# Kernel tuning notes

Hardware: AMD Instinct MI355X
Metric: run time of the kernel (lower is better)

Reference implementation:

```python
import jax, jax.numpy as jnp
import numpy as np

NUM_HEAVY = 1024
N_ITERS = 50
FETCH_K_RATIO = 9.0 / 8.0
EPS = 1.0


def rmsnorm(x, gamma):
    scale = gamma.shape[0] ** 0.5
    normed = x / jnp.maximum(jnp.linalg.norm(x, axis=-1, keepdims=True), 1e-12)
    return normed * scale * gamma


def feedforward(x, gamma, w1, b1, w2, b2):
    h = rmsnorm(x, gamma)
    h = jax.nn.gelu(h @ w1.T + b1, approximate=False)
    return h @ w2.T + b2


def coor_descent(s, n_iters, k, eps):
    # s: [b, n] router logits; faithful to lucidrains coor_descent (no mask, const eps)
    logk = jnp.log(jnp.asarray(k, s.dtype))
    a0 = jnp.zeros_like(s[..., :1])
    b0 = -s

    def body(carry, _):
        a, b = carry
        a = eps * (logk - jax.nn.logsumexp((s + b) / eps, axis=-1, keepdims=True))
        b = -jax.nn.relu(s + a)
        return (a, b), None

    (a, b), _ = jax.lax.scan(body, (a0, b0), None, length=n_iters)
    return jnp.exp((s + a + b) / eps)


def setup_inputs() -> dict:
    key = jax.random.key(0)
    ks = jax.random.split(key, 12)
    b, n, dim = 8, 8192, 1024
    d_light, d_heavy = int(dim * 0.5), dim * 4

    def lin(k, dout, din):
        bound = 1.0 / np.sqrt(din)
        k1, k2 = jax.random.split(k)
        w = jax.random.uniform(k1, (dout, din), jnp.float32, -bound, bound)
        bb = jax.random.uniform(k2, (dout,), jnp.float32, -bound, bound)
        return w, bb

    x = jax.random.normal(ks[0], (b, n, dim), jnp.float32)
    routing_token = jax.random.normal(ks[1], (dim,), jnp.float32)
    w1_l, b1_l = lin(ks[2], d_light, dim)
    w2_l, b2_l = lin(ks[3], dim, d_light)
    w1_h, b1_h = lin(ks[4], d_heavy, dim)
    w2_h, b2_h = lin(ks[5], dim, d_heavy)
    return dict(
        x=x, routing_token=routing_token,
        gamma_l=jnp.ones((dim,), jnp.float32), w1_l=w1_l, b1_l=b1_l, w2_l=w2_l, b2_l=b2_l,
        gamma_h=jnp.ones((dim,), jnp.float32), w1_h=w1_h, b1_h=b1_h, w2_h=w2_h, b2_h=b2_h,
    )


def reference(x, routing_token, gamma_l, w1_l, b1_l, w2_l, b2_l,
              gamma_h, w1_h, b1_h, w2_h, b2_h):
    b, n, dim = x.shape
    # light branch on all tokens
    light_out = feedforward(x, gamma_l, w1_l, b1_l, w2_l, b2_l)

    # router (coor_descent, num_routing_tokens=1, no mask)
    s = jnp.einsum('bnd,d->bn', x, routing_token)
    effective_k = min(NUM_HEAVY * FETCH_K_RATIO, n)
    scores = coor_descent(s, N_ITERS, effective_k, EPS)
    selected_scores, selected_indices = jax.lax.top_k(scores, NUM_HEAVY)
    # straight-through: value -> 1, grad flows through selected_scores
    selected_scores = selected_scores + jax.lax.stop_gradient(1.0 - selected_scores)

    # gather -> heavy FFN -> scale -> scatter back
    routed = jnp.take_along_axis(x, selected_indices[..., None], axis=1)  # [b, k, d]
    routed_out = feedforward(routed, gamma_h, w1_h, b1_h, w2_h, b2_h)
    routed_out = routed_out * selected_scores[..., None]

    batch_range = jnp.arange(b)[:, None]
    heavy_out = jnp.zeros_like(x).at[batch_range, selected_indices].set(routed_out)
    return light_out + heavy_out
```

## Files before the change

kernel.cpp:

```cpp
#include <hip/hip_runtime.h>
#include <cstdint>
#include <cstddef>


#define DEV __device__ __forceinline__

typedef __bf16 bf16x8 __attribute__((ext_vector_type(8)));
typedef float floatx4 __attribute__((ext_vector_type(4)));

DEV unsigned short f2bf(float f) {
  unsigned int u = __float_as_uint(f);
  u += 0x7FFFu + ((u >> 16) & 1u);
  return (unsigned short)(u >> 16);
}

__global__ __launch_bounds__(256) void convw_gamma_kernel(
    const float* __restrict__ w, const float* __restrict__ gamma,
    unsigned short* __restrict__ wb, int n) {
  int i = blockIdx.x * 256 + threadIdx.x;
  if (i < n) wb[i] = f2bf(w[i] * gamma[i & 1023]);
}
__global__ __launch_bounds__(256) void convw_kernel(
    const float* __restrict__ w, unsigned short* __restrict__ wb, int n) {
  int i = blockIdx.x * 256 + threadIdx.x;
  if (i < n) wb[i] = f2bf(w[i]);
}

__global__ __launch_bounds__(256) void prep_kernel(
    const float* __restrict__ x, const float* __restrict__ rt,
    unsigned short* __restrict__ xn, double* __restrict__ s) {
  const int token = blockIdx.x;
  const int tid = threadIdx.x;
  const float4 v = ((const float4*)(x + (size_t)token * 1024))[tid];
  const float4 r = ((const float4*)rt)[tid];
  float ss = v.x * v.x + v.y * v.y + v.z * v.z + v.w * v.w;
  double dot = (double)v.x * r.x + (double)v.y * r.y + (double)v.z * r.z + (double)v.w * r.w;
  const int wave = tid >> 6, lane = tid & 63;
#pragma unroll
  for (int off = 32; off; off >>= 1) {
    ss += __shfl_down(ss, off);
    dot += __shfl_down(dot, off);
  }
  __shared__ float ssr[4];
  __shared__ double dr[4];
  __shared__ float scale_sh;
  if (lane == 0) { ssr[wave] = ss; dr[wave] = dot; }
  __syncthreads();
  if (tid == 0) {
    float tot = ssr[0] + ssr[1] + ssr[2] + ssr[3];
    scale_sh = 32.0f / fmaxf(sqrtf(tot), 1e-12f);
    s[token] = dr[0] + dr[1] + dr[2] + dr[3];
  }
  __syncthreads();
  const float sc = scale_sh;
  ushort4 o;
  o.x = f2bf(v.x * sc); o.y = f2bf(v.y * sc);
  o.z = f2bf(v.z * sc); o.w = f2bf(v.w * sc);
  ((ushort4*)(xn + (size_t)token * 1024))[tid] = o;
}

__global__ __launch_bounds__(1024) void coor_kernel(
    const double* __restrict__ s, double* __restrict__ a_out) {
  const int b = blockIdx.x, tid = threadIdx.x;
  const int wave = tid >> 6, lane = tid & 63;
  __shared__ double red[16];
  __shared__ double bcast;
  const double* sb = s + (size_t)b * 8192;
  double sv[8], es[8];
#pragma unroll
  for (int i = 0; i < 8; ++i) {
    sv[i] = sb[tid * 8 + i];
    es[i] = exp(sv[i]);
  }
  const double logk = log(1152.0);
  double a = logk - log(8192.0);
  for (int it = 0; it < 49; ++it) {
    const double th = -a;
    const double eth = exp(th);
    double sum = 0.0;
#pragma unroll
    for (int i = 0; i < 8; ++i) sum += (sv[i] < th) ? es[i] : eth;
#pragma unroll
    for (int off = 32; off; off >>= 1) sum += __shfl_down(sum, off);
    if (lane == 0) red[wave] = sum;
    __syncthreads();
    if (tid == 0) {
      double t = 0.0;
      for (int i = 0; i < 16; ++i) t += red[i];
      bcast = logk - log(t);
    }
    __syncthreads();
    a = bcast;
  }
  if (tid == 0) a_out[b] = a;
}

__global__ __launch_bounds__(1024) void select_kernel(
    const double* __restrict__ s, const double* __restrict__ a_in,
    int* __restrict__ sel) {
  const int b = blockIdx.x, tid = threadIdx.x;
  const int wave = tid >> 6, lane = tid & 63;
  const double a = a_in[b];
  const double* sb = s + (size_t)b * 8192;
  const int base = tid * 8;
  double sv[8];
  bool ind[8];
  int cnt = 0;
#pragma unroll
  for (int i = 0; i < 8; ++i) {
    sv[i] = sb[base + i];
    ind[i] = (sv[i] + a >= 0.0);
    cnt += ind[i] ? 1 : 0;
  }
  __shared__ int sc[1024];
  sc[tid] = cnt;
  __syncthreads();
  for (int off = 1; off < 1024; off <<= 1) {
    int v = sc[tid];
    int add = (tid >= off) ? sc[tid - off] : 0;
    __syncthreads();
    sc[tid] = v + add;
    __syncthreads();
  }
  const int m = sc[1023];
  int p = sc[tid] - cnt;
#pragma unroll
  for (int i = 0; i < 8; ++i) {
    if (ind[i]) {
      if (p < 1024) sel[b * 1024 + p] = base + i;
      ++p;
    }
  }
  if (m >= 1024) return;

  __shared__ double rv[16];
  __shared__ int ri[16];
  __shared__ int gsel;
  bool taken[8] = {false, false, false, false, false, false, false, false};
  const int need = 1024 - m;
  for (int t = 0; t < need; ++t) {
    double bvv = -1.0e300;
    int bi = 0x7FFFFFFF;
#pragma unroll
    for (int i = 0; i < 8; ++i)
      if (!ind[i] && !taken[i] && sv[i] > bvv) { bvv = sv[i]; bi = base + i; }
#pragma unroll
    for (int off = 32; off; off >>= 1) {
      double ov = __shfl_down(bvv, off);
      int oi = __shfl_down(bi, off);
      if (ov > bvv || (ov == bvv && oi < bi)) { bvv = ov; bi = oi; }
    }
    if (lane == 0) { rv[wave] = bvv; ri[wave] = bi; }
    __syncthreads();
    if (tid == 0) {
      double mv = rv[0]; int mi = ri[0];
      for (int i = 1; i < 16; ++i)
        if (rv[i] > mv || (rv[i] == mv && ri[i] < mi)) { mv = rv[i]; mi = ri[i]; }
      gsel = mi;
      sel[b * 1024 + m + t] = mi;
    }
    __syncthreads();
    const int g = gsel;
    if (g >= base && g < base + 8) taken[g - base] = true;
    __syncthreads();
  }
}

__global__ __launch_bounds__(256) void gather_kernel(
    const unsigned short* __restrict__ xn, const int* __restrict__ sel,
    unsigned short* __restrict__ xg) {
  const int r = blockIdx.x;
  const int b = r >> 10;
  const int idx = sel[r];
  const uint2* src = (const uint2*)(xn + ((size_t)(b << 13) + idx) * 1024);
  uint2* dst = (uint2*)(xg + (size_t)r * 1024);
  dst[threadIdx.x] = src[threadIdx.x];
}


enum {
  RA00 = 0,      RA01 = 16384,  RA10 = 32768,  RA11 = 49152,
  RB00 = 65536,  RB01 = 81920,  RB10 = 98304,  RB11 = 114688
};

#define VMCNT(n) asm volatile("s_waitcnt vmcnt(" #n ")" ::: "memory")
#define BARR() __builtin_amdgcn_s_barrier()
#define SCHED0() __builtin_amdgcn_sched_barrier(0)

#define STG_A(DST, KOFF)                                                      \
  do {                                                                        \
    _Pragma("unroll") for (int r_ = 0; r_ < 2; ++r_)                          \
        __builtin_amdgcn_global_load_lds(                                     \
            (__attribute__((address_space(1))) void*)(Asrc[r_] + (KOFF)),     \
            (__attribute__((address_space(3))) void*)(sh + (DST) + r_ * 8192 +\
                                                     ldsW),                   \
            16, 0, 0);                                                        \
  } while (0)

#define STG_B(DST, KOFF)                                                      \
  do {                                                                        \
    _Pragma("unroll") for (int r_ = 0; r_ < 2; ++r_)                          \
        __builtin_amdgcn_global_load_lds(                                     \
            (__attribute__((address_space(1))) void*)(Bsrc[r_] + (KOFF)),     \
            (__attribute__((address_space(3))) void*)(sh + (DST) + r_ * 8192 +\
                                                     ldsW),                   \
            16, 0, 0);                                                        \
  } while (0)

#define PH(RAOFF, RBOFF, MH, LOADB, STG)                                      \
  do {                                                                        \
    bf16x8 a_[4];                                                             \
    _Pragma("unroll") for (int f_ = 0; f_ < 4; ++f_) a_[f_] =                 \
        *(const bf16x8*)(sh + (RAOFF) + f_ * 2048 + rbA);                     \
    if (LOADB) {                                                              \
      _Pragma("unroll") for (int n_ = 0; n_ < 4; ++n_) bq[n_] =               \
          *(const bf16x8*)(sh + (RBOFF) + n_ * 2048 + rbB);                   \
    }                                                                         \
    STG;                                                                      \
    __builtin_amdgcn_s_setprio(1);                                            \
    _Pragma("unroll") for (int f_ = 0; f_ < 4; ++f_)                          \
        _Pragma("unroll") for (int n_ = 0; n_ < 4; ++n_) acc[(MH) + f_][n_] = \
            __builtin_amdgcn_mfma_f32_16x16x32_bf16(a_[f_], bq[n_],           \
                                                    acc[(MH) + f_][n_], 0, 0, \
                                                    0);                       \
    __builtin_amdgcn_s_setprio(0);                                            \
  } while (0)

#define ITER_FULL(I)                                                          \
  do {                                                                        \
    const int ks4 = ((2 * (I) + 1) << 6) + 32;                                \
    const int ks1 = ((2 * (I) + 2) << 6);                                     \
    const int ks2 = ks1 + 32;                                                 \
    const int ks3 = ((2 * (I) + 3) << 6);                                     \
    PH(RA00, RB00, 0, 1, STG_A(RA11, ks4));                                   \
    PH(RA00 + 8192, RB00, 4, 0, STG_B(RB11, ks4));                            \
    VMCNT(8); BARR(); SCHED0();                                               \
    PH(RA01, RB01, 0, 1, STG_A(RA00, ks1));                                   \
    PH(RA01 + 8192, RB01, 4, 0, STG_B(RB00, ks1));                            \
    VMCNT(8); BARR(); SCHED0();                                               \
    PH(RA10, RB10, 0, 1, STG_A(RA01, ks2));                                   \
    PH(RA10 + 8192, RB10, 4, 0, STG_B(RB01, ks2));                            \
    VMCNT(8); BARR(); SCHED0();                                               \
    PH(RA11, RB11, 0, 1, STG_A(RA10, ks3));                                   \
    PH(RA11 + 8192, RB11, 4, 0, STG_B(RB10, ks3));                            \
    VMCNT(8); BARR(); SCHED0();                                               \
  } while (0)

#define ITER_LAST(I)                                                          \
  do {                                                                        \
    const int ks4 = ((2 * (I) + 1) << 6) + 32;                                \
    PH(RA00, RB00, 0, 1, STG_A(RA11, ks4));                                   \
    PH(RA00 + 8192, RB00, 4, 0, STG_B(RB11, ks4));                            \
    VMCNT(8); BARR(); SCHED0();                                               \
    PH(RA01, RB01, 0, 1, );                                                   \
    PH(RA01 + 8192, RB01, 4, 0, );                                            \
    VMCNT(4); BARR(); SCHED0();                                               \
    PH(RA10, RB10, 0, 1, );                                                   \
    PH(RA10 + 8192, RB10, 4, 0, );                                            \
    VMCNT(0); BARR(); SCHED0();                                               \
    PH(RA11, RB11, 0, 1, );                                                   \
    PH(RA11 + 8192, RB11, 4, 0, );                                            \
  } while (0)

template <int MODE>
__global__ __launch_bounds__(512, 2) void gemm8p_kernel(
    const unsigned short* __restrict__ A, const unsigned short* __restrict__ B,
    const float* __restrict__ bias, float* __restrict__ outF,
    unsigned short* __restrict__ outH, int M, int N, int K) {
  __shared__ alignas(16) char sh[131072];

  const int tiles_n = N >> 8;
  const int nwg = gridDim.x;
  const int bid = blockIdx.x;
  const int cpx = nwg >> 3;
  const int swz = (bid & 7) * cpx + (bid >> 3);
  const int bm = swz / tiles_n, bn = swz - bm * tiles_n;

  const int tid = threadIdx.x;
  const int wave = tid >> 6, lane = tid & 63;
  const int l16 = lane & 15, q = lane >> 4;
  const int wm = wave >> 2, wn = wave & 3;

  const int slA = (((wm * 4 + q) ^ (l16 & 7)) << 4);
  const int slB = ((((wn >> 1) * 4 + q) ^ (l16 & 7)) << 4);
  const int rbA = l16 * 128 + slA;
  const int rbB = (wn & 1) * 8192 + l16 * 128 + slB;

  const int ssrc = (tid & 7) ^ ((tid >> 3) & 7);
  const int hfold = ssrc >> 2, chunk = ssrc & 3;
  const unsigned short* Asrc[2];
  const unsigned short* Bsrc[2];
#pragma unroll
  for (int r = 0; r < 2; ++r) {
    const int grow = r * 64 + (tid >> 3) + hfold * 128;
    Asrc[r] = A + (size_t)(bm * 256 + grow) * K + chunk * 8;
    Bsrc[r] = B + (size_t)(bn * 256 + grow) * K + chunk * 8;
  }
  const int ldsW = wave * 1024;

  floatx4 acc[8][4];
#pragma unroll
  for (int i = 0; i < 8; ++i)
#pragma unroll
    for (int j = 0; j < 4; ++j) acc[i][j] = 0.0f;
  bf16x8 bq[4];

  STG_A(RA00, 0);  STG_B(RB00, 0);
  STG_A(RA01, 32); STG_B(RB01, 32);
  STG_A(RA10, 64); STG_B(RB10, 64);
  VMCNT(8); BARR(); SCHED0();

  const int NI = K >> 7;
#pragma unroll 1
  for (int i = 0; i < NI - 1; ++i) ITER_FULL(i);
  ITER_LAST(NI - 1);

  const int gm0 = bm * 256 + wm * 128 + q * 4;
  const int gn0 = bn * 256 + wn * 64 + l16;
#pragma unroll
  for (int m = 0; m < 8; ++m) {
#pragma unroll
    for (int n = 0; n < 4; ++n) {
      const int col = gn0 + n * 16;
      const float bv = bias[col];
#pragma unroll
      for (int r = 0; r < 4; ++r) {
        const int row = gm0 + m * 16 + r;
        float v = acc[m][n][r] + bv;
        if (MODE == 0) {
          float g = 0.5f * v * (1.0f + erff(v * 0.70710678118654752f));
          outH[(size_t)row * N + col] = f2bf(g);
        } else {
          outF[(size_t)row * N + col] = v;
        }
      }
    }
  }
}

template <int MODE>
__global__ __launch_bounds__(256, 3) void gemm_bt_kernel(
    const unsigned short* __restrict__ A, const unsigned short* __restrict__ B,
    const float* __restrict__ bias, float* __restrict__ outF,
    unsigned short* __restrict__ outH, const int* __restrict__ sel,
    int M, int N, int K) {
  constexpr int BK = 32;
  __shared__ alignas(16) unsigned short As[128 * BK];
  __shared__ alignas(16) unsigned short Bs[128 * BK];
  const int tiles_n = N >> 7;
  int bid = blockIdx.x;
  if ((gridDim.x & 7) == 0) {
    bid = (bid & 7) * (gridDim.x >> 3) + (bid >> 3);
  }
  const int bm = bid / tiles_n;
  const int bn = bid - bm * tiles_n;
  const int tid = threadIdx.x;
  const int wave = tid >> 6, lane = tid & 63;
  const int quad = lane >> 4, l16 = lane & 15;
  const int wm = (wave >> 1) << 6;
  const int wn = (wave & 1) << 6;

  floatx4 acc[4][4];
#pragma unroll
  for (int i = 0; i < 4; ++i)
#pragma unroll
    for (int j = 0; j < 4; ++j) acc[i][j] = 0.0f;

  const int sr = tid >> 2;
  const int scol = (tid & 3) << 3;
  const unsigned short* Ag = A + ((size_t)(bm * 128 + sr)) * K + scol;
  const unsigned short* Bg = B + ((size_t)(bn * 128 + sr)) * K + scol;
  const size_t rowstep = (size_t)64 * K;
  char* AsB = (char*)&As[0];
  char* BsB = (char*)&Bs[0];
  const int ldsbase = wave * 1024;

  for (int k0 = 0; k0 < K; k0 += BK) {
#pragma unroll
    for (int iss = 0; iss < 2; ++iss) {
      __builtin_amdgcn_global_load_lds(
          (__attribute__((address_space(1))) void*)(Ag + iss * rowstep + k0),
          (__attribute__((address_space(3))) void*)(AsB + ldsbase + iss * 4096), 16, 0, 0);
      __builtin_amdgcn_global_load_lds(
          (__attribute__((address_space(1))) void*)(Bg + iss * rowstep + k0),
          (__attribute__((address_space(3))) void*)(BsB + ldsbase + iss * 4096), 16, 0, 0);
    }
    __syncthreads();
    bf16x8 af[4], bfr[4];
#pragma unroll
    for (int mi = 0; mi < 4; ++mi)
      af[mi] = *(const bf16x8*)(As + (wm + mi * 16 + l16) * BK + quad * 8);
#pragma unroll
    for (int ni = 0; ni < 4; ++ni)
      bfr[ni] = *(const bf16x8*)(Bs + (wn + ni * 16 + l16) * BK + quad * 8);
#pragma unroll
    for (int mi = 0; mi < 4; ++mi)
#pragma unroll
      for (int ni = 0; ni < 4; ++ni)
        acc[mi][ni] = __builtin_amdgcn_mfma_f32_16x16x32_bf16(af[mi], bfr[ni], acc[mi][ni], 0, 0, 0);
    __syncthreads();
  }

  const int gm0 = bm * 128 + wm + quad * 4;
  const int gn0 = bn * 128 + wn + l16;
#pragma unroll
  for (int mi = 0; mi < 4; ++mi) {
#pragma unroll
    for (int ni = 0; ni < 4; ++ni) {
      const int col = gn0 + ni * 16;
      const float bv = bias[col];
#pragma unroll
      for (int r = 0; r < 4; ++r) {
        const int row = gm0 + mi * 16 + r;
        float v = acc[mi][ni][r] + bv;
        if (MODE == 0) {
          float g = 0.5f * v * (1.0f + erff(v * 0.70710678118654752f));
          outH[(size_t)row * N + col] = f2bf(g);
        } else if (MODE == 1) {
          outF[(size_t)row * N + col] = v;
        } else {
          const int idx = sel[row];
          const size_t op = (((size_t)((row >> 10) << 13) + idx) << 10) + col;
          outF[op] += v;
        }
      }
    }
  }
}

extern "C" void kernel_launch(void* const* d_in, const int* in_sizes, int n_in,
                              void* d_out, int out_size, void* d_ws, size_t ws_size,
                              hipStream_t stream) {
  const float* x    = (const float*)d_in[0];
  const float* rt   = (const float*)d_in[1];
  const float* g_l  = (const float*)d_in[2];
  const float* w1_l = (const float*)d_in[3];
  const float* b1_l = (const float*)d_in[4];
  const float* w2_l = (const float*)d_in[5];
  const float* b2_l = (const float*)d_in[6];
  const float* g_h  = (const float*)d_in[7];
  const float* w1_h = (const float*)d_in[8];
  const float* b1_h = (const float*)d_in[9];
  const float* w2_h = (const float*)d_in[10];
  const float* b2_h = (const float*)d_in[11];
  float* out = (float*)d_out;

  char* ws = (char*)d_ws;
  size_t off = 0;
  auto alloc = [&](size_t bytes) -> char* {
    char* p = ws + off;
    off += (bytes + 255) & ~(size_t)255;
    return p;
  };
  unsigned short* xn  = (unsigned short*)alloc((size_t)65536 * 1024 * 2);
  double* s           = (double*)alloc((size_t)65536 * 8);
  double* a_out       = (double*)alloc(256);
  int* sel            = (int*)alloc(8192 * 4);
  unsigned short* w1l = (unsigned short*)alloc((size_t)512 * 1024 * 2);
  unsigned short* w2l = (unsigned short*)alloc((size_t)1024 * 512 * 2);
  unsigned short* w1h = (unsigned short*)alloc((size_t)4096 * 1024 * 2);
  unsigned short* w2h = (unsigned short*)alloc((size_t)1024 * 4096 * 2);
  unsigned short* xg  = (unsigned short*)alloc((size_t)8192 * 1024 * 2);
  unsigned short* h1  = (unsigned short*)alloc((size_t)33554432 * 2);
  if (off > ws_size) return;

  convw_gamma_kernel<<<524288 / 256, 256, 0, stream>>>(w1_l, g_l, w1l, 524288);
  convw_kernel<<<524288 / 256, 256, 0, stream>>>(w2_l, w2l, 524288);
  convw_gamma_kernel<<<4194304 / 256, 256, 0, stream>>>(w1_h, g_h, w1h, 4194304);
  convw_kernel<<<4194304 / 256, 256, 0, stream>>>(w2_h, w2h, 4194304);

  prep_kernel<<<65536, 256, 0, stream>>>(x, rt, xn, s);
  coor_kernel<<<8, 1024, 0, stream>>>(s, a_out);
  select_kernel<<<8, 1024, 0, stream>>>(s, a_out, sel);
  gather_kernel<<<8192, 256, 0, stream>>>(xn, sel, xg);

  gemm8p_kernel<0><<<256 * 2, 512, 0, stream>>>(xn, w1l, b1_l, nullptr, h1, 65536, 512, 1024);
  gemm8p_kernel<1><<<256 * 4, 512, 0, stream>>>(h1, w2l, b2_l, out, nullptr, 65536, 1024, 512);
  gemm8p_kernel<0><<<32 * 16, 512, 0, stream>>>(xg, w1h, b1_h, nullptr, h1, 8192, 4096, 1024);
  gemm_bt_kernel<2><<<64 * 8, 256, 0, stream>>>(h1, w2h, b2_h, out, nullptr, sel, 8192, 1024, 4096);
}
```

Baseline: 951.6 us.

## Fuse gather into heavy GEMM, split-K heavy down-proj, merge heavy output into light epilogue

The heavy branch now loads its selected token rows straight from xn through per-row gathered A pointers, so the separate gather kernel goes away. The heavy down-projection moves from the slow 128-tile kernel to the pipelined 256-tile kernel with a 2-way split-K into two fp32 buffers. The light second GEMM's epilogue then adds those partials using an inverse selection map, replacing the read-modify-write scatter and reordering the branches. This costs extra global traffic for the fp32 partials and an invsel write per token.

```diff
diff --git a/kernel.cpp b/kernel.cpp
--- a/kernel.cpp
+++ b/kernel.cpp
@@ -97,7 +97,7 @@
 
 __global__ __launch_bounds__(1024) void select_kernel(
     const double* __restrict__ s, const double* __restrict__ a_in,
-    int* __restrict__ sel) {
+    int* __restrict__ sel, int* __restrict__ invsel) {
   const int b = blockIdx.x, tid = threadIdx.x;
   const int wave = tid >> 6, lane = tid & 63;
   const double a = a_in[b];
@@ -126,10 +126,12 @@
   int p = sc[tid] - cnt;
 #pragma unroll
   for (int i = 0; i < 8; ++i) {
+    int w = -1;
     if (ind[i]) {
-      if (p < 1024) sel[b * 1024 + p] = base + i;
+      if (p < 1024) { sel[b * 1024 + p] = base + i; w = p; }
       ++p;
     }
+    invsel[b * 8192 + base + i] = w;
   }
   if (m >= 1024) return;
 
@@ -158,23 +160,13 @@
         if (rv[i] > mv || (rv[i] == mv && ri[i] < mi)) { mv = rv[i]; mi = ri[i]; }
       gsel = mi;
       sel[b * 1024 + m + t] = mi;
+      invsel[b * 8192 + mi] = m + t;
     }
     __syncthreads();
     const int g = gsel;
     if (g >= base && g < base + 8) taken[g - base] = true;
     __syncthreads();
   }
-}
-
-__global__ __launch_bounds__(256) void gather_kernel(
-    const unsigned short* __restrict__ xn, const int* __restrict__ sel,
-    unsigned short* __restrict__ xg) {
-  const int r = blockIdx.x;
-  const int b = r >> 10;
-  const int idx = sel[r];
-  const uint2* src = (const uint2*)(xn + ((size_t)(b << 13) + idx) * 1024);
-  uint2* dst = (uint2*)(xg + (size_t)r * 1024);
-  dst[threadIdx.x] = src[threadIdx.x];
 }
 
 
@@ -262,11 +254,13 @@
     PH(RA11 + 8192, RB11, 4, 0, );                                            \
   } while (0)
 
-template <int MODE>
+template <int MODE, bool SELA>
 __global__ __launch_bounds__(512, 2) void gemm8p_kernel(
     const unsigned short* __restrict__ A, const unsigned short* __restrict__ B,
     const float* __restrict__ bias, float* __restrict__ outF,
-    unsigned short* __restrict__ outH, int M, int N, int K) {
+    unsigned short* __restrict__ outH, const int* __restrict__ sel,
+    const float* __restrict__ hA, const float* __restrict__ hB,
+    float* __restrict__ outF2, int M, int N, int K) {
   __shared__ alignas(16) char sh[131072];
 
   const int tiles_n = N >> 8;
@@ -274,7 +268,12 @@
   const int bid = blockIdx.x;
   const int cpx = nwg >> 3;
   const int swz = (bid & 7) * cpx + (bid >> 3);
-  const int bm = swz / tiles_n, bn = swz - bm * tiles_n;
+
+  int tile = swz, ksplit = 0;
+  if (MODE == 3) { ksplit = swz >= (nwg >> 1); tile = swz & ((nwg >> 1) - 1); }
+  const int Kloop = (MODE == 3) ? (K >> 1) : K;
+  const int kbase = (MODE == 3) ? ksplit * (K >> 1) : 0;
+  const int bm = tile / tiles_n, bn = tile - bm * tiles_n;
 
   const int tid = threadIdx.x;
   const int wave = tid >> 6, lane = tid & 63;
@@ -292,9 +291,15 @@
   const unsigned short* Bsrc[2];
 #pragma unroll
   for (int r = 0; r < 2; ++r) {
-    const int grow = r * 64 + (tid >> 3) + hfold * 128;
-    Asrc[r] = A + (size_t)(bm * 256 + grow) * K + chunk * 8;
-    Bsrc[r] = B + (size_t)(bn * 256 + grow) * K + chunk * 8;
+    const int growA = bm * 256 + r * 64 + (tid >> 3) + hfold * 128;
+    const int growB = bn * 256 + r * 64 + (tid >> 3) + hfold * 128;
+    if (SELA) {
+      const int bb = growA >> 10;
+      Asrc[r] = A + ((size_t)((bb << 13) + sel[growA])) * K + kbase + chunk * 8;
+    } else {
+      Asrc[r] = A + (size_t)growA * K + kbase + chunk * 8;
+    }
+    Bsrc[r] = B + (size_t)growB * K + kbase + chunk * 8;
   }
   const int ldsW = wave * 1024;
 
@@ -310,19 +315,20 @@
   STG_A(RA10, 64); STG_B(RB10, 64);
   VMCNT(8); BARR(); SCHED0();
 
-  const int NI = K >> 7;
+  const int NI = Kloop >> 7;
 #pragma unroll 1
   for (int i = 0; i < NI - 1; ++i) ITER_FULL(i);
   ITER_LAST(NI - 1);
 
   const int gm0 = bm * 256 + wm * 128 + q * 4;
   const int gn0 = bn * 256 + wn * 64 + l16;
+  float* const oF = (MODE == 3 && ksplit) ? outF2 : outF;
 #pragma unroll
   for (int m = 0; m < 8; ++m) {
 #pragma unroll
     for (int n = 0; n < 4; ++n) {
       const int col = gn0 + n * 16;
-      const float bv = bias[col];
+      const float bv = (MODE == 3 && ksplit) ? 0.0f : bias[col];
 #pragma unroll
       for (int r = 0; r < 4; ++r) {
         const int row = gm0 + m * 16 + r;
@@ -330,98 +336,15 @@
         if (MODE == 0) {
           float g = 0.5f * v * (1.0f + erff(v * 0.70710678118654752f));
           outH[(size_t)row * N + col] = f2bf(g);
-        } else {
-          outF[(size_t)row * N + col] = v;
-        }
-      }
-    }
-  }
-}
-
-template <int MODE>
-__global__ __launch_bounds__(256, 3) void gemm_bt_kernel(
-    const unsigned short* __restrict__ A, const unsigned short* __restrict__ B,
-    const float* __restrict__ bias, float* __restrict__ outF,
-    unsigned short* __restrict__ outH, const int* __restrict__ sel,
-    int M, int N, int K) {
-  constexpr int BK = 32;
-  __shared__ alignas(16) unsigned short As[128 * BK];
-  __shared__ alignas(16) unsigned short Bs[128 * BK];
-  const int tiles_n = N >> 7;
-  int bid = blockIdx.x;
-  if ((gridDim.x & 7) == 0) {
-    bid = (bid & 7) * (gridDim.x >> 3) + (bid >> 3);
-  }
-  const int bm = bid / tiles_n;
-  const int bn = bid - bm * tiles_n;
-  const int tid = threadIdx.x;
-  const int wave = tid >> 6, lane = tid & 63;
-  const int quad = lane >> 4, l16 = lane & 15;
-  const int wm = (wave >> 1) << 6;
-  const int wn = (wave & 1) << 6;
-
-  floatx4 acc[4][4];
-#pragma unroll
-  for (int i = 0; i < 4; ++i)
-#pragma unroll
-    for (int j = 0; j < 4; ++j) acc[i][j] = 0.0f;
-
-  const int sr = tid >> 2;
-  const int scol = (tid & 3) << 3;
-  const unsigned short* Ag = A + ((size_t)(bm * 128 + sr)) * K + scol;
-  const unsigned short* Bg = B + ((size_t)(bn * 128 + sr)) * K + scol;
-  const size_t rowstep = (size_t)64 * K;
-  char* AsB = (char*)&As[0];
-  char* BsB = (char*)&Bs[0];
-  const int ldsbase = wave * 1024;
-
-  for (int k0 = 0; k0 < K; k0 += BK) {
-#pragma unroll
-    for (int iss = 0; iss < 2; ++iss) {
-      __builtin_amdgcn_global_load_lds(
-          (__attribute__((address_space(1))) void*)(Ag + iss * rowstep + k0),
-          (__attribute__((address_space(3))) void*)(AsB + ldsbase + iss * 4096), 16, 0, 0);
-      __builtin_amdgcn_global_load_lds(
-          (__attribute__((address_space(1))) void*)(Bg + iss * rowstep + k0),
-          (__attribute__((address_space(3))) void*)(BsB + ldsbase + iss * 4096), 16, 0, 0);
-    }
-    __syncthreads();
-    bf16x8 af[4], bfr[4];
-#pragma unroll
-    for (int mi = 0; mi < 4; ++mi)
-      af[mi] = *(const bf16x8*)(As + (wm + mi * 16 + l16) * BK + quad * 8);
-#pragma unroll
-    for (int ni = 0; ni < 4; ++ni)
-      bfr[ni] = *(const bf16x8*)(Bs + (wn + ni * 16 + l16) * BK + quad * 8);
-#pragma unroll
-    for (int mi = 0; mi < 4; ++mi)
-#pragma unroll
-      for (int ni = 0; ni < 4; ++ni)
-        acc[mi][ni] = __builtin_amdgcn_mfma_f32_16x16x32_bf16(af[mi], bfr[ni], acc[mi][ni], 0, 0, 0);
-    __syncthreads();
-  }
-
-  const int gm0 = bm * 128 + wm + quad * 4;
-  const int gn0 = bn * 128 + wn + l16;
-#pragma unroll
-  for (int mi = 0; mi < 4; ++mi) {
-#pragma unroll
-    for (int ni = 0; ni < 4; ++ni) {
-      const int col = gn0 + ni * 16;
-      const float bv = bias[col];
-#pragma unroll
-      for (int r = 0; r < 4; ++r) {
-        const int row = gm0 + mi * 16 + r;
-        float v = acc[mi][ni][r] + bv;
-        if (MODE == 0) {
-          float g = 0.5f * v * (1.0f + erff(v * 0.70710678118654752f));
-          outH[(size_t)row * N + col] = f2bf(g);
-        } else if (MODE == 1) {
+        } else if (MODE == 2) {
+          const int slot = sel[row];
+          if (slot >= 0) {
+            const size_t hrow = (((size_t)(row >> 13)) << 10) + slot;
+            v += hA[(hrow << 10) + col] + hB[(hrow << 10) + col];
+          }
           outF[(size_t)row * N + col] = v;
         } else {
-          const int idx = sel[row];
-          const size_t op = (((size_t)((row >> 10) << 13) + idx) << 10) + col;
-          outF[op] += v;
+          oF[(size_t)row * N + col] = v;
         }
       }
     }
@@ -456,12 +379,14 @@
   double* s           = (double*)alloc((size_t)65536 * 8);
   double* a_out       = (double*)alloc(256);
   int* sel            = (int*)alloc(8192 * 4);
+  int* invsel         = (int*)alloc((size_t)65536 * 4);
   unsigned short* w1l = (unsigned short*)alloc((size_t)512 * 1024 * 2);
   unsigned short* w2l = (unsigned short*)alloc((size_t)1024 * 512 * 2);
   unsigned short* w1h = (unsigned short*)alloc((size_t)4096 * 1024 * 2);
   unsigned short* w2h = (unsigned short*)alloc((size_t)1024 * 4096 * 2);
-  unsigned short* xg  = (unsigned short*)alloc((size_t)8192 * 1024 * 2);
   unsigned short* h1  = (unsigned short*)alloc((size_t)33554432 * 2);
+  float* hA           = (float*)alloc((size_t)8192 * 1024 * 4);
+  float* hB           = (float*)alloc((size_t)8192 * 1024 * 4);
   if (off > ws_size) return;
 
   convw_gamma_kernel<<<524288 / 256, 256, 0, stream>>>(w1_l, g_l, w1l, 524288);
@@ -471,11 +396,14 @@
 
   prep_kernel<<<65536, 256, 0, stream>>>(x, rt, xn, s);
   coor_kernel<<<8, 1024, 0, stream>>>(s, a_out);
-  select_kernel<<<8, 1024, 0, stream>>>(s, a_out, sel);
-  gather_kernel<<<8192, 256, 0, stream>>>(xn, sel, xg);
-
-  gemm8p_kernel<0><<<256 * 2, 512, 0, stream>>>(xn, w1l, b1_l, nullptr, h1, 65536, 512, 1024);
-  gemm8p_kernel<1><<<256 * 4, 512, 0, stream>>>(h1, w2l, b2_l, out, nullptr, 65536, 1024, 512);
-  gemm8p_kernel<0><<<32 * 16, 512, 0, stream>>>(xg, w1h, b1_h, nullptr, h1, 8192, 4096, 1024);
-  gemm_bt_kernel<2><<<64 * 8, 256, 0, stream>>>(h1, w2h, b2_h, out, nullptr, sel, 8192, 1024, 4096);
-}
+  select_kernel<<<8, 1024, 0, stream>>>(s, a_out, sel, invsel);
+
+  gemm8p_kernel<0, true><<<512, 512, 0, stream>>>(
+      xn, w1h, b1_h, nullptr, h1, sel, nullptr, nullptr, nullptr, 8192, 4096, 1024);
+  gemm8p_kernel<3, false><<<256, 512, 0, stream>>>(
+      h1, w2h, b2_h, hA, nullptr, nullptr, nullptr, nullptr, hB, 8192, 1024, 4096);
+  gemm8p_kernel<0, false><<<512, 512, 0, stream>>>(
+      xn, w1l, b1_l, nullptr, h1, nullptr, nullptr, nullptr, nullptr, 65536, 512, 1024);
+  gemm8p_kernel<2, false><<<1024, 512, 0, stream>>>(
+      h1, w2l, b2_l, out, nullptr, invsel, hA, hB, nullptr, 65536, 1024, 512);
+}
```

After: 1.017 ms. +6.9%, slower.
